# Kernel tuning notes

Measured on AMD Instinct MI355X. Metric: run time of the kernel, lower is better.

The kernel has to match this reference:

```python
import jax, jax.numpy as jnp
import numpy as np

B, S, E, H = 4, 1024, 1024, 16
HD = E // H
TEMP = float(E) ** 0.5


def setup_inputs() -> dict:
    key = jax.random.key(0)
    ks = jax.random.split(key, 6)
    x = jax.random.normal(ks[0], (B, S, E), dtype=jnp.float32)
    mask = jax.random.randint(ks[1], (1, 1, S, S), 0, 2).astype(bool)
    prev = jax.random.normal(ks[2], (B, H, S, S), dtype=jnp.float32)
    qkv_w = jax.random.normal(ks[3], (3 * E, E), dtype=jnp.float32) * (1.0 / np.sqrt(E))
    qkv_b = jnp.zeros((3 * E,), dtype=jnp.float32)
    o_w = jax.random.normal(ks[4], (E, E), dtype=jnp.float32) * (1.0 / np.sqrt(E))
    o_b = jnp.zeros((E,), dtype=jnp.float32)
    return {"x": x, "mask": mask, "prev": prev, "qkv_w": qkv_w,
            "qkv_b": qkv_b, "o_w": o_w, "o_b": o_b}


def reference(x, mask, prev, qkv_w, qkv_b, o_w, o_b):
    b, s, _ = x.shape
    # qkv_proj: torch Linear -> x @ W^T + b, then per-head interleaved split
    qkv = x @ qkv_w.T + qkv_b                      # [B, S, 3E]
    qkv = qkv.reshape(b, s, H, 3 * HD).transpose(0, 2, 1, 3)  # [B, H, S, 3*HD]
    q, k, v = jnp.split(qkv, 3, axis=-1)           # each [B, H, S, HD]
    attn = jnp.einsum('bhqd,bhkd->bhqk', q, k) / TEMP + prev  # raw scores
    attn = jnp.where(mask, -jnp.inf, attn)         # masked_fill(mask, -inf)
    p = jax.nn.softmax(attn, axis=-1)              # dropout p=0 (eval)
    vals = jnp.einsum('bhqk,bhkd->bhqd', p, v)     # [B, H, S, HD]
    vals = vals.transpose(0, 2, 1, 3).reshape(b, s, E)
    return vals @ o_w.T + o_b
```

## Files before the change

kernel.cpp:

```cpp
#include <hip/hip_runtime.h>

typedef unsigned short u16;
typedef unsigned char  u8;
typedef unsigned long long u64;

using bf16x8 = __attribute__((ext_vector_type(8))) short;
using f32x4  = __attribute__((ext_vector_type(4))) float;

static __device__ __forceinline__ u16 f2bf(float f) {
  union { float f; unsigned u; } v; v.f = f;
  unsigned r = v.u + 0x7fffu + ((v.u >> 16) & 1u);
  return (u16)(r >> 16);
}

static __device__ __forceinline__ void gload_lds16(const void* g, void* l) {
  __builtin_amdgcn_global_load_lds((const __attribute__((address_space(1))) void*)g,
                                   (__attribute__((address_space(3))) void*)l, 16, 0, 0);
}

__global__ __launch_bounds__(256) void cvt_bf16_kernel(const float4* __restrict__ in,
                                                       ushort4* __restrict__ out, int n4) {
  int i = blockIdx.x * 256 + threadIdx.x;
  if (i >= n4) return;
  float4 v = in[i];
  ushort4 o;
  o.x = f2bf(v.x); o.y = f2bf(v.y); o.z = f2bf(v.z); o.w = f2bf(v.w);
  out[i] = o;
}

__global__ __launch_bounds__(256) void zero_out_kernel(float* __restrict__ out, int n) {
  int i = blockIdx.x * 256 + threadIdx.x;
  if (i < n) out[i] = 0.f;
}

__global__ __launch_bounds__(256) void mask_pack_kernel(const void* __restrict__ mask,
                                                        u64* __restrict__ out) {
  __shared__ int nz;
  const int tid = threadIdx.x, b = blockIdx.x;
  if (tid == 0) nz = 0;
  __syncthreads();
  const int idx = b * 256 + tid;
  const u8 byte = ((const u8*)mask)[idx];
  if ((idx & 3) && byte) atomicAdd(&nz, 1);
  __syncthreads();
  int m;
  if (nz == 0) m = ((const int*)mask)[idx] != 0;
  else         m = byte != 0;
  u64 bits = __ballot(m);
  if ((tid & 63) == 0) out[b * 4 + (tid >> 6)] = bits;
}

template<bool OUT_BF16>
__global__ __launch_bounds__(256, 2)
void gemm_bt(const u16* __restrict__ A, const u16* __restrict__ Bm,
             const float* __restrict__ bias, void* __restrict__ Cout,
             int M, int N, int K) {
  constexpr int BK = 64;
  __shared__ u16 lA[128 * BK];
  __shared__ u16 lB[128 * BK];
  const int tid = threadIdx.x;
  const int wv = tid >> 6, lane = tid & 63;
  const int wr = (wv >> 1) * 64, wc = (wv & 1) * 64;
  const int bm = blockIdx.x * 128, bn = blockIdx.y * 128;
  const int frow = lane & 15, fk = (lane >> 4) * 8;
  const int srow = tid >> 3;
  const int scol = (tid & 7) * 8;
  const u16* ga = A + (size_t)(bm + srow) * K + scol;
  const u16* gb = Bm + (size_t)(bn + srow) * K + scol;
  u16* la = &lA[srow * BK + scol];
  u16* lb = &lB[srow * BK + scol];

  f32x4 acc[4][4] = {};

  for (int k0 = 0; k0 < K; k0 += BK) {
#pragma unroll
    for (int r = 0; r < 4; ++r) {
      gload_lds16(ga + (size_t)(r * 32) * K + k0, la + r * 32 * BK);
      gload_lds16(gb + (size_t)(r * 32) * K + k0, lb + r * 32 * BK);
    }
    __syncthreads();
#pragma unroll
    for (int kk = 0; kk < 2; ++kk) {
      bf16x8 af[4], bf[4];
#pragma unroll
      for (int m = 0; m < 4; ++m)
        af[m] = *(const bf16x8*)&lA[(wr + m * 16 + frow) * BK + kk * 32 + fk];
#pragma unroll
      for (int n = 0; n < 4; ++n)
        bf[n] = *(const bf16x8*)&lB[(wc + n * 16 + frow) * BK + kk * 32 + fk];
#pragma unroll
      for (int m = 0; m < 4; ++m)
#pragma unroll
        for (int n = 0; n < 4; ++n)
          acc[m][n] = __builtin_amdgcn_mfma_f32_16x16x32_bf16(af[m], bf[n], acc[m][n], 0, 0, 0);
    }
    __syncthreads();
  }
#pragma unroll
  for (int n = 0; n < 4; ++n) {
    const int col = bn + wc + n * 16 + frow;
    const float bv = bias[col];
#pragma unroll
    for (int m = 0; m < 4; ++m) {
      const int row0 = bm + wr + m * 16 + (lane >> 4) * 4;
#pragma unroll
      for (int r = 0; r < 4; ++r) {
        float v = acc[m][n][r] + bv;
        if constexpr (OUT_BF16)
          ((u16*)Cout)[(size_t)(row0 + r) * N + col] = f2bf(v);
        else
          ((float*)Cout)[(size_t)(row0 + r) * N + col] = v;
      }
    }
  }
}

__global__ __launch_bounds__(256, 3)
void attn_kernel(const u16* __restrict__ qkv,
                 const float* __restrict__ prev,
                 const u64* __restrict__ mbits,
                 u16* __restrict__ vals) {
  constexpr int S = 1024;
  __shared__ u16 lQ[64 * 64];
  __shared__ u16 lK[64 * 64];
  __shared__ u16 lVT[64 * 64];
  __shared__ u16 lP[4][16 * 72];
  __shared__ float lPrev[64 * 64];
  const int tid = threadIdx.x, wv = tid >> 6, lane = tid & 63;
  const int bh = blockIdx.x >> 4;
  const int qt = blockIdx.x & 15;
  const int b = bh >> 4, h = bh & 15;
  const int frow = lane & 15, fkg = lane >> 4, fk = fkg * 8;
  const int srow = tid >> 3, scol8 = (tid & 7) * 8;
  const size_t rowQ0 = (size_t)(b * S + qt * 64);

  const int scol_sw = scol8 ^ ((srow & 7) << 3);
  const int c0 = fk ^ ((frow & 7) << 3);
  const int c1 = (fk + 32) ^ ((frow & 7) << 3);

  {
    const u16* g = qkv + (rowQ0 + srow) * 3072 + h * 192 + scol_sw;
    gload_lds16(g, &lQ[srow * 64 + scol8]);
    gload_lds16(g + (size_t)32 * 3072, &lQ[(srow + 32) * 64 + scol8]);
  }
  __syncthreads();
  bf16x8 qf0 = *(const bf16x8*)&lQ[(wv * 16 + frow) * 64 + c0];
  bf16x8 qf1 = *(const bf16x8*)&lQ[(wv * 16 + frow) * 64 + c1];

  float m_run[4], l_run[4];
  f32x4 acc_o[4] = {};
#pragma unroll
  for (int r = 0; r < 4; ++r) { m_run[r] = -3e38f; l_run[r] = 0.f; }

  const int qloc = wv * 16 + fkg * 4;
  const u64* mrow = mbits + (size_t)(qt * 64 + qloc) * (S / 64);

  const float* prevt = prev + ((size_t)bh * S + qt * 64) * S;
  const int prow_s = wv * 4 + (lane >> 4);
  const int pcolg = ((lane & 15) * 4) ^ (wv << 4);
  const int prd = fkg << 4;

  const int vsw = (tid & 7) << 3;

  for (int kt = 0; kt < 16; ++kt) {
    __syncthreads();
    const u16* gv = qkv + (size_t)(b * S + kt * 64 + srow) * 3072 + h * 192 + 128 + scol8;
    bf16x8 v0 = *(const bf16x8*)gv;
    bf16x8 v1 = *(const bf16x8*)(gv + (size_t)32 * 3072);
    {
      const u16* g = qkv + (size_t)(b * S + kt * 64 + srow) * 3072 + h * 192 + 64 + scol_sw;
      gload_lds16(g, &lK[srow * 64 + scol8]);
      gload_lds16(g + (size_t)32 * 3072, &lK[(srow + 32) * 64 + scol8]);
    }
    {
      const float* p0 = prevt + (size_t)kt * 64 + pcolg;
#pragma unroll
      for (int i = 0; i < 4; ++i)
        gload_lds16(p0 + (size_t)(i * 16 + prow_s) * S, &lPrev[(i * 256 + tid) * 4]);
    }
    {
      const int k0 = srow ^ vsw;
      const int k1 = (srow + 32) ^ vsw;
#pragma unroll
      for (int j = 0; j < 8; ++j) {
        lVT[(scol8 + j) * 64 + k0] = (u16)v0[j];
        lVT[(scol8 + j) * 64 + k1] = (u16)v1[j];
      }
    }
    __syncthreads();
    u64 mw[4];
#pragma unroll
    for (int r = 0; r < 4; ++r) mw[r] = mrow[r * (S / 64) + kt];
    f32x4 s[4];
#pragma unroll
    for (int n = 0; n < 4; ++n) {
      bf16x8 kf0 = *(const bf16x8*)&lK[(n * 16 + frow) * 64 + c0];
      bf16x8 kf1 = *(const bf16x8*)&lK[(n * 16 + frow) * 64 + c1];
      f32x4 z = {0.f, 0.f, 0.f, 0.f};
      z = __builtin_amdgcn_mfma_f32_16x16x32_bf16(qf0, kf0, z, 0, 0, 0);
      s[n] = __builtin_amdgcn_mfma_f32_16x16x32_bf16(qf1, kf1, z, 0, 0, 0);
    }
#pragma unroll
    for (int r = 0; r < 4; ++r) {
      const u64 t = mw[r] >> frow;
      const int prbase = (qloc + r) * 64;
#pragma unroll
      for (int n = 0; n < 4; ++n) {
        float pv = lPrev[prbase + ((n * 16 + frow) ^ prd)];
        float sc = s[n][r] * 0.03125f + pv;
        s[n][r] = ((t >> (n * 16)) & 1ull) ? -1e30f : sc;
      }
    }
    float tmax[4];
#pragma unroll
    for (int r = 0; r < 4; ++r) {
      float t = fmaxf(fmaxf(s[0][r], s[1][r]), fmaxf(s[2][r], s[3][r]));
      t = fmaxf(t, __shfl_xor(t, 1));
      t = fmaxf(t, __shfl_xor(t, 2));
      t = fmaxf(t, __shfl_xor(t, 4));
      t = fmaxf(t, __shfl_xor(t, 8));
      tmax[r] = t;
    }
    float psum[4];
#pragma unroll
    for (int r = 0; r < 4; ++r) {
      float mnew = fmaxf(m_run[r], tmax[r]);
      float sc = __expf(m_run[r] - mnew);
      m_run[r] = mnew;
      l_run[r] *= sc;
#pragma unroll
      for (int dn = 0; dn < 4; ++dn) acc_o[dn][r] *= sc;
      float ps = 0.f;
#pragma unroll
      for (int n = 0; n < 4; ++n) {
        float p = __expf(s[n][r] - mnew);
        s[n][r] = p;
        ps += p;
      }
      psum[r] = ps;
    }
#pragma unroll
    for (int r = 0; r < 4; ++r) {
      float t = psum[r];
      t += __shfl_xor(t, 1); t += __shfl_xor(t, 2);
      t += __shfl_xor(t, 4); t += __shfl_xor(t, 8);
      l_run[r] += t;
    }
    u16* pw = &lP[wv][0];
#pragma unroll
    for (int n = 0; n < 4; ++n)
#pragma unroll
      for (int r = 0; r < 4; ++r)
        pw[(fkg * 4 + r) * 72 + n * 16 + frow] = f2bf(s[n][r]);
    bf16x8 pf0 = *(const bf16x8*)&pw[frow * 72 + fk];
    bf16x8 pf1 = *(const bf16x8*)&pw[frow * 72 + 32 + fk];
#pragma unroll
    for (int dn = 0; dn < 4; ++dn) {
      const int d = dn * 16 + frow;
      const int sw = ((dn * 2 + (frow >> 3)) & 7) << 3;
      bf16x8 vt0 = *(const bf16x8*)&lVT[d * 64 + (fk ^ sw)];
      bf16x8 vt1 = *(const bf16x8*)&lVT[d * 64 + ((fk + 32) ^ sw)];
      acc_o[dn] = __builtin_amdgcn_mfma_f32_16x16x32_bf16(pf0, vt0, acc_o[dn], 0, 0, 0);
      acc_o[dn] = __builtin_amdgcn_mfma_f32_16x16x32_bf16(pf1, vt1, acc_o[dn], 0, 0, 0);
    }
  }
#pragma unroll
  for (int r = 0; r < 4; ++r) {
    float inv = 1.0f / l_run[r];
    size_t row = (rowQ0 + qloc + r) * 1024 + h * 64;
#pragma unroll
    for (int dn = 0; dn < 4; ++dn)
      vals[row + dn * 16 + frow] = f2bf(acc_o[dn][r] * inv);
  }
}

extern "C" void kernel_launch(void* const* d_in, const int* in_sizes, int n_in,
                              void* d_out, int out_size, void* d_ws, size_t ws_size,
                              hipStream_t stream) {
  const float* x     = (const float*)d_in[0];
  const void*  mask  = d_in[1];
  const float* prev  = (const float*)d_in[2];
  const float* qkv_w = (const float*)d_in[3];
  const float* qkv_b = (const float*)d_in[4];
  const float* o_w   = (const float*)d_in[5];
  const float* o_b   = (const float*)d_in[6];

  const size_t WS_NEEDED = 41943040 + 131072;
  if (ws_size < WS_NEEDED) {
    zero_out_kernel<<<(out_size + 255) / 256, 256, 0, stream>>>((float*)d_out, out_size);
    return;
  }

  char* ws = (char*)d_ws;
  u16* x_bf  = (u16*)(ws);
  u16* vals  = (u16*)(ws);
  u16* qw_bf = (u16*)(ws + 8388608);
  u16* ow_bf = (u16*)(ws + 8388608);
  u16* qkv_o = (u16*)(ws + 14680064);
  u64* mask_b = (u64*)(ws + 41943040);

  mask_pack_kernel<<<4096, 256, 0, stream>>>(mask, mask_b);
  cvt_bf16_kernel<<<4096, 256, 0, stream>>>((const float4*)x, (ushort4*)x_bf, 1048576);
  cvt_bf16_kernel<<<3072, 256, 0, stream>>>((const float4*)qkv_w, (ushort4*)qw_bf, 786432);

  dim3 g1(32, 24);
  gemm_bt<true><<<g1, 256, 0, stream>>>(x_bf, qw_bf, qkv_b, qkv_o, 4096, 3072, 1024);

  cvt_bf16_kernel<<<1024, 256, 0, stream>>>((const float4*)o_w, (ushort4*)ow_bf, 262144);

  attn_kernel<<<1024, 256, 0, stream>>>(qkv_o, prev, mask_b, vals);

  dim3 g2(32, 8);
  gemm_bt<false><<<g2, 256, 0, stream>>>(vals, ow_bf, o_b, d_out, 4096, 1024, 1024);
}
```

Measured before the change: 517.9 us.

## Double-buffer K/V tiles and prefetch prev scores directly into registers

```diff
diff --git a/kernel.cpp b/kernel.cpp
--- a/kernel.cpp
+++ b/kernel.cpp
@@ -122,10 +122,9 @@
                  u16* __restrict__ vals) {
   constexpr int S = 1024;
   __shared__ u16 lQ[64 * 64];
-  __shared__ u16 lK[64 * 64];
-  __shared__ u16 lVT[64 * 64];
+  __shared__ u16 lK[2][64 * 64];
+  __shared__ u16 lVT[2][64 * 64];
   __shared__ u16 lP[4][16 * 72];
-  __shared__ float lPrev[64 * 64];
   const int tid = threadIdx.x, wv = tid >> 6, lane = tid & 63;
   const int bh = blockIdx.x >> 4;
   const int qt = blockIdx.x & 15;
@@ -137,13 +136,45 @@
   const int scol_sw = scol8 ^ ((srow & 7) << 3);
   const int c0 = fk ^ ((frow & 7) << 3);
   const int c1 = (fk + 32) ^ ((frow & 7) << 3);
+  const int vsw = (tid & 7) << 3;
+
+  const int qloc = wv * 16 + fkg * 4;
+  const u64* mrow = mbits + (size_t)(qt * 64 + qloc) * (S / 64);
+  const float* prow = prev + ((size_t)bh * S + qt * 64 + qloc) * S;
 
   {
     const u16* g = qkv + (rowQ0 + srow) * 3072 + h * 192 + scol_sw;
     gload_lds16(g, &lQ[srow * 64 + scol8]);
     gload_lds16(g + (size_t)32 * 3072, &lQ[(srow + 32) * 64 + scol8]);
   }
+  {
+    const u16* g = qkv + (size_t)(b * S + srow) * 3072 + h * 192 + 64 + scol_sw;
+    gload_lds16(g, &lK[0][srow * 64 + scol8]);
+    gload_lds16(g + (size_t)32 * 3072, &lK[0][(srow + 32) * 64 + scol8]);
+  }
+  bf16x8 v0, v1;
+  {
+    const u16* gv = qkv + (size_t)(b * S + srow) * 3072 + h * 192 + 128 + scol8;
+    v0 = *(const bf16x8*)gv;
+    v1 = *(const bf16x8*)(gv + (size_t)32 * 3072);
+    const int k0 = srow ^ vsw, k1 = (srow + 32) ^ vsw;
+#pragma unroll
+    for (int j = 0; j < 8; ++j) {
+      lVT[0][(scol8 + j) * 64 + k0] = (u16)v0[j];
+      lVT[0][(scol8 + j) * 64 + k1] = (u16)v1[j];
+    }
+  }
+  float pvraw[4][4];
+  u64 mw[4];
+#pragma unroll
+  for (int r = 0; r < 4; ++r) mw[r] = mrow[r * (S / 64)];
+#pragma unroll
+  for (int n = 0; n < 4; ++n)
+#pragma unroll
+    for (int r = 0; r < 4; ++r)
+      pvraw[n][r] = prow[(size_t)r * S + n * 16 + frow];
   __syncthreads();
+
   bf16x8 qf0 = *(const bf16x8*)&lQ[(wv * 16 + frow) * 64 + c0];
   bf16x8 qf1 = *(const bf16x8*)&lQ[(wv * 16 + frow) * 64 + c1];
 
@@ -152,50 +183,22 @@
 #pragma unroll
   for (int r = 0; r < 4; ++r) { m_run[r] = -3e38f; l_run[r] = 0.f; }
 
-  const int qloc = wv * 16 + fkg * 4;
-  const u64* mrow = mbits + (size_t)(qt * 64 + qloc) * (S / 64);
-
-  const float* prevt = prev + ((size_t)bh * S + qt * 64) * S;
-  const int prow_s = wv * 4 + (lane >> 4);
-  const int pcolg = ((lane & 15) * 4) ^ (wv << 4);
-  const int prd = fkg << 4;
-
-  const int vsw = (tid & 7) << 3;
-
   for (int kt = 0; kt < 16; ++kt) {
-    __syncthreads();
-    const u16* gv = qkv + (size_t)(b * S + kt * 64 + srow) * 3072 + h * 192 + 128 + scol8;
-    bf16x8 v0 = *(const bf16x8*)gv;
-    bf16x8 v1 = *(const bf16x8*)(gv + (size_t)32 * 3072);
-    {
-      const u16* g = qkv + (size_t)(b * S + kt * 64 + srow) * 3072 + h * 192 + 64 + scol_sw;
-      gload_lds16(g, &lK[srow * 64 + scol8]);
-      gload_lds16(g + (size_t)32 * 3072, &lK[(srow + 32) * 64 + scol8]);
-    }
-    {
-      const float* p0 = prevt + (size_t)kt * 64 + pcolg;
-#pragma unroll
-      for (int i = 0; i < 4; ++i)
-        gload_lds16(p0 + (size_t)(i * 16 + prow_s) * S, &lPrev[(i * 256 + tid) * 4]);
-    }
-    {
-      const int k0 = srow ^ vsw;
-      const int k1 = (srow + 32) ^ vsw;
-#pragma unroll
-      for (int j = 0; j < 8; ++j) {
-        lVT[(scol8 + j) * 64 + k0] = (u16)v0[j];
-        lVT[(scol8 + j) * 64 + k1] = (u16)v1[j];
-      }
-    }
-    __syncthreads();
-    u64 mw[4];
-#pragma unroll
-    for (int r = 0; r < 4; ++r) mw[r] = mrow[r * (S / 64) + kt];
+    const int cur = kt & 1;
+    const bool more = (kt < 15);
+    if (more) {
+      const u16* g = qkv + (size_t)(b * S + (kt + 1) * 64 + srow) * 3072 + h * 192 + 64 + scol_sw;
+      gload_lds16(g, &lK[cur ^ 1][srow * 64 + scol8]);
+      gload_lds16(g + (size_t)32 * 3072, &lK[cur ^ 1][(srow + 32) * 64 + scol8]);
+      const u16* gv = qkv + (size_t)(b * S + (kt + 1) * 64 + srow) * 3072 + h * 192 + 128 + scol8;
+      v0 = *(const bf16x8*)gv;
+      v1 = *(const bf16x8*)(gv + (size_t)32 * 3072);
+    }
     f32x4 s[4];
 #pragma unroll
     for (int n = 0; n < 4; ++n) {
-      bf16x8 kf0 = *(const bf16x8*)&lK[(n * 16 + frow) * 64 + c0];
-      bf16x8 kf1 = *(const bf16x8*)&lK[(n * 16 + frow) * 64 + c1];
+      bf16x8 kf0 = *(const bf16x8*)&lK[cur][(n * 16 + frow) * 64 + c0];
+      bf16x8 kf1 = *(const bf16x8*)&lK[cur][(n * 16 + frow) * 64 + c1];
       f32x4 z = {0.f, 0.f, 0.f, 0.f};
       z = __builtin_amdgcn_mfma_f32_16x16x32_bf16(qf0, kf0, z, 0, 0, 0);
       s[n] = __builtin_amdgcn_mfma_f32_16x16x32_bf16(qf1, kf1, z, 0, 0, 0);
@@ -203,13 +206,21 @@
 #pragma unroll
     for (int r = 0; r < 4; ++r) {
       const u64 t = mw[r] >> frow;
-      const int prbase = (qloc + r) * 64;
 #pragma unroll
       for (int n = 0; n < 4; ++n) {
-        float pv = lPrev[prbase + ((n * 16 + frow) ^ prd)];
-        float sc = s[n][r] * 0.03125f + pv;
+        float sc = s[n][r] * 0.03125f + pvraw[n][r];
         s[n][r] = ((t >> (n * 16)) & 1ull) ? -1e30f : sc;
       }
+    }
+    if (more) {
+#pragma unroll
+      for (int r = 0; r < 4; ++r) mw[r] = mrow[r * (S / 64) + kt + 1];
+      const float* pp = prow + (kt + 1) * 64 + frow;
+#pragma unroll
+      for (int n = 0; n < 4; ++n)
+#pragma unroll
+        for (int r = 0; r < 4; ++r)
+          pvraw[n][r] = pp[(size_t)r * S + n * 16];
     }
     float tmax[4];
 #pragma unroll
@@ -246,6 +257,14 @@
       t += __shfl_xor(t, 4); t += __shfl_xor(t, 8);
       l_run[r] += t;
     }
+    if (more) {
+      const int k0 = srow ^ vsw, k1 = (srow + 32) ^ vsw;
+#pragma unroll
+      for (int j = 0; j < 8; ++j) {
+        lVT[cur ^ 1][(scol8 + j) * 64 + k0] = (u16)v0[j];
+        lVT[cur ^ 1][(scol8 + j) * 64 + k1] = (u16)v1[j];
+      }
+    }
     u16* pw = &lP[wv][0];
 #pragma unroll
     for (int n = 0; n < 4; ++n)
@@ -258,11 +277,12 @@
     for (int dn = 0; dn < 4; ++dn) {
       const int d = dn * 16 + frow;
       const int sw = ((dn * 2 + (frow >> 3)) & 7) << 3;
-      bf16x8 vt0 = *(const bf16x8*)&lVT[d * 64 + (fk ^ sw)];
-      bf16x8 vt1 = *(const bf16x8*)&lVT[d * 64 + ((fk + 32) ^ sw)];
+      bf16x8 vt0 = *(const bf16x8*)&lVT[cur][d * 64 + (fk ^ sw)];
+      bf16x8 vt1 = *(const bf16x8*)&lVT[cur][d * 64 + ((fk + 32) ^ sw)];
       acc_o[dn] = __builtin_amdgcn_mfma_f32_16x16x32_bf16(pf0, vt0, acc_o[dn], 0, 0, 0);
       acc_o[dn] = __builtin_amdgcn_mfma_f32_16x16x32_bf16(pf1, vt1, acc_o[dn], 0, 0, 0);
     }
+    __syncthreads();
   }
 #pragma unroll
   for (int r = 0; r < 4; ++r) {
```

New measurement: 500.6 us. 3.4% less time.
